# Performance work log

Hardware: AMD Instinct MI355X
Metric: run time of the kernel (lower is better)

Reference implementation:

```python
import jax, jax.numpy as jnp
import numpy as np

N, S, T, E, H = 4, 2048, 2048, 512, 8
HD = E // H  # head_dim = 64


def setup_inputs() -> dict:
    key0 = jax.random.key(0)
    ks = jax.random.split(key0, 12)
    sc = 1.0 / np.sqrt(E)
    inp = {
        "query": jax.random.normal(ks[0], (N, S, E), jnp.float32),
        "key": jax.random.normal(ks[1], (N, T, E), jnp.float32),
        "value": jax.random.normal(ks[2], (N, T, E), jnp.float32),
        "attn_mask": jnp.tril(jnp.ones((S, T), jnp.int32)),  # causal: 0 => masked
        # nn.Linear weights (out, in) and biases, torch convention y = x @ W.T + b
        "Wq": jax.random.normal(ks[3], (E, E), jnp.float32) * sc,
        "bq": jax.random.normal(ks[4], (E,), jnp.float32) * sc,
        "Wk": jax.random.normal(ks[5], (E, E), jnp.float32) * sc,
        "bk": jax.random.normal(ks[6], (E,), jnp.float32) * sc,
        "Wv": jax.random.normal(ks[7], (E, E), jnp.float32) * sc,
        "bv": jax.random.normal(ks[8], (E,), jnp.float32) * sc,
        "Wp": jax.random.normal(ks[9], (E, E), jnp.float32) * sc,
        "bp": jax.random.normal(ks[10], (E,), jnp.float32) * sc,
    }
    return inp


def reference(query, key, value, attn_mask, Wq, bq, Wk, bk, Wv, bv, Wp, bp):
    # QKV projections, split heads: (N, H, L, HD)
    q = (query @ Wq.T + bq).reshape(N, S, H, HD).transpose(0, 2, 1, 3)
    k = (key @ Wk.T + bk).reshape(N, T, H, HD).transpose(0, 2, 1, 3)
    v = (value @ Wv.T + bv).reshape(N, T, H, HD).transpose(0, 2, 1, 3)
    # scaled scores (N, H, S, T) -- intentionally materialized like the original
    e = jnp.einsum("nhsd,nhtd->nhst", q, k) / jnp.sqrt(jnp.float32(HD))
    e = jnp.where(attn_mask == 0, -jnp.inf, e)
    a = jax.nn.softmax(e, axis=-1)
    # dropout is identity in eval mode (reference runs deterministic/eval)
    y = jnp.einsum("nhst,nhtd->nhsd", a, v)
    y = y.transpose(0, 2, 1, 3).reshape(N, S, E)
    return y @ Wp.T + bp
```

## Files before the change

kernel.cpp:

```cpp
#include <hip/hip_runtime.h>


#define DEV __device__ __forceinline__

typedef unsigned short u16;
typedef unsigned int u32;
typedef __bf16 bf16x8 __attribute__((ext_vector_type(8)));
typedef float f32x4 __attribute__((ext_vector_type(4)));
typedef float f32x16 __attribute__((ext_vector_type(16)));

#define MFMA16(A, B, C) __builtin_amdgcn_mfma_f32_16x16x32_bf16(A, B, C, 0, 0, 0)
#define MFMA32(A, B, C) __builtin_amdgcn_mfma_f32_32x32x16_bf16(A, B, C, 0, 0, 0)

#define SC 0.18033688f

DEV u16 f2bf(float f) {
  u32 u = __builtin_bit_cast(u32, f);
  u += 0x7fffu + ((u >> 16) & 1u);
  return (u16)(u >> 16);
}
DEV u32 pk2(float lo, float hi) {
  u32 a = __builtin_bit_cast(u32, lo) + 0x8000u;
  u32 b = __builtin_bit_cast(u32, hi) + 0x8000u;
  return __builtin_amdgcn_perm(b, a, 0x07060302u);
}

DEV void cp16(void* l, const void* g) {
  __builtin_amdgcn_global_load_lds(
      (const __attribute__((address_space(1))) u32*)g,
      (__attribute__((address_space(3))) u32*)l, 16, 0, 0);
}

__global__ __launch_bounds__(256) void cast_all(
    const float* __restrict__ q, const float* __restrict__ k, const float* __restrict__ v,
    const float* __restrict__ wq, const float* __restrict__ wk, const float* __restrict__ wv,
    const float* __restrict__ wp,
    u16* qo, u16* ko, u16* vo, u16* wqo, u16* wko, u16* wvo, u16* wpo) {
  int b = blockIdx.x, tid = threadIdx.x;
  const float* s;
  u16* d;
  int off;
  float sc = 1.f;
  if (b < 12288) {
    int which = b >> 12;
    s = (which == 0) ? q : (which == 1) ? k : v;
    d = (which == 0) ? qo : (which == 1) ? ko : vo;
    off = (b & 4095) * 256;
  } else {
    int wb = b - 12288, which = wb >> 8;
    s = (which == 0) ? wq : (which == 1) ? wk : (which == 2) ? wv : wp;
    d = (which == 0) ? wqo : (which == 1) ? wko : (which == 2) ? wvo : wpo;
    off = (wb & 255) * 256;
    if (which == 0) sc = SC;
  }
  int i = off + tid;
  float4 f = ((const float4*)s)[i];
  ushort4 o;
  o.x = f2bf(f.x * sc); o.y = f2bf(f.y * sc); o.z = f2bf(f.z * sc); o.w = f2bf(f.w * sc);
  ((ushort4*)d)[i] = o;
}

DEV void gemm_loop(const u16* __restrict__ A, const u16* __restrict__ W,
                   u16* As, u16* Bs, int m0, int n0, int tid, f32x4 acc[4][4]) {
  const int lane = tid & 63, wid = tid >> 6;
  const int wm = wid & 1, wn = wid >> 1;
  const int l15 = lane & 15, l4 = lane >> 4;
  for (int kt = 0; kt < 512; kt += 32) {
    __syncthreads();
#pragma unroll
    for (int i = 0; i < 2; ++i) {
      int c = tid + 256 * i;
      int row = c >> 2, kc = (c & 3) * 8;
      cp16(&As[c * 8], A + (m0 + row) * 512 + kt + kc);
      cp16(&Bs[c * 8], W + (n0 + row) * 512 + kt + kc);
    }
    __syncthreads();
    bf16x8 af[4], bfr[4];
#pragma unroll
    for (int f = 0; f < 4; ++f) {
      af[f]  = *(const bf16x8*)&As[(wm * 64 + f * 16 + l15) * 32 + l4 * 8];
      bfr[f] = *(const bf16x8*)&Bs[(wn * 64 + f * 16 + l15) * 32 + l4 * 8];
    }
#pragma unroll
    for (int fm = 0; fm < 4; ++fm)
#pragma unroll
      for (int fn = 0; fn < 4; ++fn)
        acc[fm][fn] = MFMA16(af[fm], bfr[fn], acc[fm][fn]);
  }
}

__global__ __launch_bounds__(256) void gemm_qkv(
    const u16* __restrict__ qx, const u16* __restrict__ kx, const u16* __restrict__ vx,
    const u16* __restrict__ wq, const u16* __restrict__ wk, const u16* __restrict__ wv,
    const float* __restrict__ bq, const float* __restrict__ bk, const float* __restrict__ bv,
    u16* qp, u16* kp, u16* vt) {
  __shared__ u16 As[128 * 32];
  __shared__ u16 Bs[128 * 32];
  const int wsel = blockIdx.x >> 2;
  const int xq = blockIdx.x & 3;
  const u16* A = (wsel == 0) ? qx : (wsel == 1) ? kx : wv;
  const u16* W = (wsel == 0) ? wq : (wsel == 1) ? wk : vx;
  const float* bias = (wsel == 0) ? bq : (wsel == 1) ? bk : bv;
  const int m0 = (wsel == 2) ? xq * 128 : blockIdx.y * 128;
  const int n0 = (wsel == 2) ? blockIdx.y * 128 : xq * 128;
  const int tid = threadIdx.x, lane = tid & 63, wid = tid >> 6;
  const int wm = wid & 1, wn = wid >> 1;
  const int l15 = lane & 15, l4 = lane >> 4;

  f32x4 acc[4][4] = {};
  gemm_loop(A, W, As, Bs, m0, n0, tid, acc);

  if (wsel < 2) {
    u16* C = (wsel == 0) ? qp : kp;
    const float bscale = (wsel == 0) ? SC : 1.f;
#pragma unroll
    for (int fn = 0; fn < 4; ++fn) {
      int col = n0 + wn * 64 + fn * 16 + l15;
      float bvv = bias[col] * bscale;
#pragma unroll
      for (int fm = 0; fm < 4; ++fm) {
        int rowb = m0 + wm * 64 + fm * 16 + l4 * 4;
#pragma unroll
        for (int r = 0; r < 4; ++r)
          C[(rowb + r) * 512 + col] = f2bf(acc[fm][fn][r] + bvv);
      }
    }
  } else {
    const int nIdx = n0 >> 11;
    const int tb = n0 & 2047;
#pragma unroll
    for (int fm = 0; fm < 4; ++fm) {
      int rowb = m0 + wm * 64 + fm * 16 + l4 * 4;
#pragma unroll
      for (int r = 0; r < 4; ++r) {
        int row = rowb + r;
        float bvv = bias[row];
        int vtrow = (nIdx * 8 + (row >> 6)) * 64 + (row & 63);
#pragma unroll
        for (int fn = 0; fn < 4; ++fn) {
          int tcol = tb + wn * 64 + fn * 16 + l15;
          vt[vtrow * 2048 + tcol] = f2bf(acc[fm][fn][r] + bvv);
        }
      }
    }
  }
}

__global__ __launch_bounds__(256) void gemm_out(const u16* __restrict__ A,
                                                const u16* __restrict__ W,
                                                const float* __restrict__ bias,
                                                float* __restrict__ C) {
  __shared__ u16 As[128 * 32];
  __shared__ u16 Bs[128 * 32];
  const int n0 = blockIdx.x * 128, m0 = blockIdx.y * 128;
  const int tid = threadIdx.x, lane = tid & 63, wid = tid >> 6;
  const int wm = wid & 1, wn = wid >> 1;
  const int l15 = lane & 15, l4 = lane >> 4;

  f32x4 acc[4][4] = {};
  gemm_loop(A, W, As, Bs, m0, n0, tid, acc);

#pragma unroll
  for (int fn = 0; fn < 4; ++fn) {
    int col = n0 + wn * 64 + fn * 16 + l15;
    float bvv = bias[col];
#pragma unroll
    for (int fm = 0; fm < 4; ++fm) {
      int rowb = m0 + wm * 64 + fm * 16 + l4 * 4;
#pragma unroll
      for (int r = 0; r < 4; ++r)
        C[(rowb + r) * 512 + col] = acc[fm][fn][r] + bvv;
    }
  }
}

__global__ __launch_bounds__(128, 4) void attn_partial(
    const u16* __restrict__ Qg, const u16* __restrict__ Kg, const u16* __restrict__ Vt,
    u16* __restrict__ scrO, float* __restrict__ scrL) {
  __shared__ u16 Ks[128 * 64];
  __shared__ u16 Vs[64 * 128];

  const int nh = blockIdx.x;
  const int yy = blockIdx.y;
  const int qt = 31 - (yy >> 2), c = yy & 3;
  if (c > (qt >> 3)) return;
  const int n = nh >> 3, h = nh & 7;
  const int tid = threadIdx.x, lane = tid & 63, w = tid >> 6;
  const int l31 = lane & 31, lh = lane >> 5;
  const int s0 = qt * 64;
  const int ntiles = (qt >> 1) + 1;
  const int it0 = c * 4, it1 = min(it0 + 4, ntiles);

  const u16* Qb = Qg + (n * 2048 + s0) * 512 + h * 64;
  const u16* Kb = Kg + n * 2048 * 512 + h * 64;
  const u16* Vb = Vt + nh * 64 * 2048;

#pragma unroll
  for (int i = 0; i < 4; ++i) {
    int ci = tid + 128 * i;
    int m = ci >> 3, pc = ci & 7;
    cp16(&Ks[ci * 8], Qb + m * 512 + ((pc ^ (m & 7)) * 8));
  }
  __syncthreads();
  const int qm = w * 32 + l31;
  bf16x8 qf[4];
#pragma unroll
  for (int ks = 0; ks < 4; ++ks)
    qf[ks] = *(const bf16x8*)&Ks[qm * 64 + (((2 * ks + lh) ^ (qm & 7)) * 8)];

  f32x16 accO[2] = {};
  float lrow = 0.f;

  for (int it = it0; it < it1; ++it) {
    const int t0 = it * 128;
    __syncthreads();
#pragma unroll
    for (int i = 0; i < 8; ++i) {
      int ci = tid + 128 * i;
      int t = ci >> 3, pc = ci & 7;
      cp16(&Ks[ci * 8], Kb + (t0 + t) * 512 + ((pc ^ (t & 7)) * 8));
    }
#pragma unroll
    for (int i = 0; i < 8; ++i) {
      int ci = tid + 128 * i;
      int d = ci >> 4, pc = ci & 15;
      cp16(&Vs[ci * 8], Vb + d * 2048 + t0 + ((pc ^ (d & 15)) * 8));
    }
    __syncthreads();

    const bool diag = (it == ntiles - 1);
    const int nf = diag ? min(4, ((s0 + 32 * w + 31 - t0) >> 5) + 1) : 4;

#pragma unroll
    for (int f = 0; f < 4; ++f)
      if (f < nf) {
        f32x16 a = {};
        int tr = f * 32 + l31;
#pragma unroll
        for (int ks = 0; ks < 4; ++ks) {
          bf16x8 kf = *(const bf16x8*)&Ks[tr * 64 + (((2 * ks + lh) ^ (tr & 7)) * 8)];
          a = MFMA32(kf, qf[ks], a);
        }
        if (diag) {
#pragma unroll
          for (int rr = 0; rr < 16; ++rr) {
            int trow = t0 + f * 32 + (rr & 3) + 8 * (rr >> 2) + 4 * lh;
            a[rr] = (trow > s0 + qm) ? -1e30f : a[rr];
          }
        }
        u32 pd[8];
#pragma unroll
        for (int rr = 0; rr < 16; ++rr) {
          float pv = __builtin_amdgcn_exp2f(a[rr]);
          a[rr] = pv;
          lrow += pv;
        }
#pragma unroll
        for (int g = 0; g < 4; ++g) {
          pd[2 * g]     = pk2(a[4 * g + 0], a[4 * g + 1]);
          pd[2 * g + 1] = pk2(a[4 * g + 2], a[4 * g + 3]);
        }
#pragma unroll
        for (int hh = 0; hh < 2; ++hh) {
          u32 ss0 = lh ? pd[4 * hh + 0] : pd[4 * hh + 2];
          u32 ss1 = lh ? pd[4 * hh + 1] : pd[4 * hh + 3];
          u32 r0 = __shfl_xor(ss0, 32);
          u32 r1 = __shfl_xor(ss1, 32);
          uint4 b4;
          b4.x = lh ? r0 : pd[4 * hh + 0];
          b4.y = lh ? r1 : pd[4 * hh + 1];
          b4.z = lh ? pd[4 * hh + 2] : r0;
          b4.w = lh ? pd[4 * hh + 3] : r1;
          bf16x8 pb = __builtin_bit_cast(bf16x8, b4);
          const int ks = 2 * f + hh;
#pragma unroll
          for (int fd = 0; fd < 2; ++fd) {
            int d = fd * 32 + l31;
            bf16x8 vf = *(const bf16x8*)&Vs[d * 128 + (((2 * ks + lh) ^ (d & 15)) * 8)];
            accO[fd] = MFMA32(vf, pb, accO[fd]);
          }
        }
      }
  }

  lrow += __shfl_xor(lrow, 32);
  const int slot = ((nh << 5) + qt) * 4 + c;
  if (lh == 0) scrL[slot * 64 + qm] = lrow;
  u16* so = scrO + slot * 4096 + qm * 64;
#pragma unroll
  for (int fd = 0; fd < 2; ++fd)
#pragma unroll
    for (int g = 0; g < 4; ++g) {
      ushort4 o;
      o.x = f2bf(accO[fd][4 * g + 0]);
      o.y = f2bf(accO[fd][4 * g + 1]);
      o.z = f2bf(accO[fd][4 * g + 2]);
      o.w = f2bf(accO[fd][4 * g + 3]);
      *(ushort4*)(so + fd * 32 + 8 * g + 4 * lh) = o;
    }
}

__global__ __launch_bounds__(128) void attn_combine(const u16* __restrict__ scrO,
                                                    const float* __restrict__ scrL,
                                                    u16* __restrict__ y) {
  const int nh = blockIdx.x, qt = blockIdx.y;
  const int n = nh >> 3, h = nh & 7;
  const int nc = (qt >> 3) + 1;
  const int tid = threadIdx.x;
  const int m = tid >> 1, half = tid & 1;

  float o[32];
#pragma unroll
  for (int j = 0; j < 32; ++j) o[j] = 0.f;
  float lsum = 0.f;
  for (int cs = 0; cs < nc; ++cs) {
    int base = ((nh << 5) + qt) * 4 + cs;
    lsum += scrL[base * 64 + m];
    const uint4* p = (const uint4*)(scrO + base * 4096 + m * 64 + half * 32);
#pragma unroll
    for (int k2 = 0; k2 < 4; ++k2) {
      uint4 qv = p[k2];
      u32 ua[4] = {qv.x, qv.y, qv.z, qv.w};
#pragma unroll
      for (int j = 0; j < 4; ++j) {
        o[k2 * 8 + 2 * j]     += __builtin_bit_cast(float, ua[j] << 16);
        o[k2 * 8 + 2 * j + 1] += __builtin_bit_cast(float, ua[j] & 0xFFFF0000u);
      }
    }
  }
  float inv = 1.f / lsum;
  u16* yb = y + (n * 2048 + qt * 64 + m) * 512 + h * 64 + half * 32;
#pragma unroll
  for (int k2 = 0; k2 < 4; ++k2) {
    uint4 ov;
    ov.x = (u32)f2bf(o[k2 * 8 + 0] * inv) | ((u32)f2bf(o[k2 * 8 + 1] * inv) << 16);
    ov.y = (u32)f2bf(o[k2 * 8 + 2] * inv) | ((u32)f2bf(o[k2 * 8 + 3] * inv) << 16);
    ov.z = (u32)f2bf(o[k2 * 8 + 4] * inv) | ((u32)f2bf(o[k2 * 8 + 5] * inv) << 16);
    ov.w = (u32)f2bf(o[k2 * 8 + 6] * inv) | ((u32)f2bf(o[k2 * 8 + 7] * inv) << 16);
    *(uint4*)(yb + k2 * 8) = ov;
  }
}

extern "C" void kernel_launch(void* const* d_in, const int* in_sizes, int n_in,
                              void* d_out, int out_size, void* d_ws, size_t ws_size,
                              hipStream_t stream) {
  (void)in_sizes; (void)n_in; (void)out_size; (void)ws_size;
  const float* query = (const float*)d_in[0];
  const float* key_  = (const float*)d_in[1];
  const float* value = (const float*)d_in[2];
  const float* Wq = (const float*)d_in[4];
  const float* bq = (const float*)d_in[5];
  const float* Wk = (const float*)d_in[6];
  const float* bk = (const float*)d_in[7];
  const float* Wv = (const float*)d_in[8];
  const float* bv = (const float*)d_in[9];
  const float* Wp = (const float*)d_in[10];
  const float* bp = (const float*)d_in[11];

  char* ws = (char*)d_ws;
  u16* qx  = (u16*)(ws);
  u16* kx  = (u16*)(ws + 8388608);
  u16* vx  = (u16*)(ws + 16777216);
  u16* scrO = (u16*)(ws);
  u16* wqx = (u16*)(ws + 33554432);
  u16* wkx = (u16*)(ws + 34078720);
  u16* wvx = (u16*)(ws + 34603008);
  u16* wpx = (u16*)(ws + 35127296);
  u16* qp  = (u16*)(ws + 35651584);
  u16* kp  = (u16*)(ws + 44040192);
  u16* vt  = (u16*)(ws + 52428800);
  u16* y   = (u16*)(ws + 60817408);
  float* scrL = (float*)(ws + 69206016);

  cast_all<<<13312, 256, 0, stream>>>(query, key_, value, Wq, Wk, Wv, Wp,
                                      qx, kx, vx, wqx, wkx, wvx, wpx);
  gemm_qkv<<<dim3(12, 64), 256, 0, stream>>>(qx, kx, vx, wqx, wkx, wvx,
                                             bq, bk, bv, qp, kp, vt);
  attn_partial<<<dim3(32, 128), 128, 0, stream>>>(qp, kp, vt, scrO, scrL);
  attn_combine<<<dim3(32, 32), 128, 0, stream>>>(scrO, scrL, y);
  gemm_out<<<dim3(4, 64), 256, 0, stream>>>(y, wpx, bp, (float*)d_out);
}
```

Measured before the change: 215.9 us.

## Double-buffer K/V tiles and enlarge query tile to 128 rows in attention

The attention partial kernel now handles 128 query rows with 4 waves (256 threads), so each K/V tile loaded into shared memory is reused by twice as many queries. It double-buffers K/V in shared memory, prefetching the next tile while the current one is computed, and drops the second barrier per iteration. Block indexing is compacted so no empty blocks are launched, and the combine kernel is adjusted to the new slot layout. In exchange, shared memory per block grows to 64KB and there are fewer blocks, which may lower occupancy.

After: 213.1 us. Within noise of the previous version (-1.3%).

```diff
diff --git a/kernel.cpp b/kernel.cpp
--- a/kernel.cpp
+++ b/kernel.cpp
@@ -174,21 +174,23 @@
   }
 }
 
-__global__ __launch_bounds__(128, 4) void attn_partial(
+__global__ __launch_bounds__(256) void attn_partial(
     const u16* __restrict__ Qg, const u16* __restrict__ Kg, const u16* __restrict__ Vt,
     u16* __restrict__ scrO, float* __restrict__ scrL) {
-  __shared__ u16 Ks[128 * 64];
-  __shared__ u16 Vs[64 * 128];
+  __shared__ u16 KV[2][16384];
 
   const int nh = blockIdx.x;
-  const int yy = blockIdx.y;
-  const int qt = 31 - (yy >> 2), c = yy & 3;
-  if (c > (qt >> 3)) return;
+  const int j = blockIdx.y;
+  int qt, c;
+  if (j < 16)      { qt = 12 + (j >> 2); c = j & 3; }
+  else if (j < 28) { int r = j - 16; int q3 = r / 3; qt = 8 + q3; c = r - 3 * q3; }
+  else if (j < 36) { int r = j - 28; qt = 4 + (r >> 1); c = r & 1; }
+  else             { qt = j - 36; c = 0; }
   const int n = nh >> 3, h = nh & 7;
   const int tid = threadIdx.x, lane = tid & 63, w = tid >> 6;
   const int l31 = lane & 31, lh = lane >> 5;
-  const int s0 = qt * 64;
-  const int ntiles = (qt >> 1) + 1;
+  const int s0 = qt * 128;
+  const int ntiles = qt + 1;
   const int it0 = c * 4, it1 = min(it0 + 4, ntiles);
 
   const u16* Qb = Qg + (n * 2048 + s0) * 512 + h * 64;
@@ -197,39 +199,61 @@
 
 #pragma unroll
   for (int i = 0; i < 4; ++i) {
-    int ci = tid + 128 * i;
+    int ci = tid + 256 * i;
     int m = ci >> 3, pc = ci & 7;
-    cp16(&Ks[ci * 8], Qb + m * 512 + ((pc ^ (m & 7)) * 8));
+    cp16(&KV[1][ci * 8], Qb + m * 512 + ((pc ^ (m & 7)) * 8));
   }
   __syncthreads();
   const int qm = w * 32 + l31;
   bf16x8 qf[4];
 #pragma unroll
   for (int ks = 0; ks < 4; ++ks)
-    qf[ks] = *(const bf16x8*)&Ks[qm * 64 + (((2 * ks + lh) ^ (qm & 7)) * 8)];
+    qf[ks] = *(const bf16x8*)&KV[1][qm * 64 + (((2 * ks + lh) ^ (qm & 7)) * 8)];
+
+  {
+    const int t0 = it0 * 128;
+#pragma unroll
+    for (int i = 0; i < 4; ++i) {
+      int ci = tid + 256 * i;
+      int t = ci >> 3, pc = ci & 7;
+      cp16(&KV[0][ci * 8], Kb + (t0 + t) * 512 + ((pc ^ (t & 7)) * 8));
+    }
+#pragma unroll
+    for (int i = 0; i < 4; ++i) {
+      int ci = tid + 256 * i;
+      int d = ci >> 4, pc = ci & 15;
+      cp16(&KV[0][8192 + ci * 8], Vb + d * 2048 + t0 + ((pc ^ (d & 15)) * 8));
+    }
+  }
 
   f32x16 accO[2] = {};
   float lrow = 0.f;
 
   for (int it = it0; it < it1; ++it) {
+    const int b = (it - it0) & 1;
+    __syncthreads();
+    if (it + 1 < it1) {
+      const int t0n = (it + 1) * 128;
+      u16* Kd = KV[b ^ 1];
+      u16* Vd = KV[b ^ 1] + 8192;
+#pragma unroll
+      for (int i = 0; i < 4; ++i) {
+        int ci = tid + 256 * i;
+        int t = ci >> 3, pc = ci & 7;
+        cp16(&Kd[ci * 8], Kb + (t0n + t) * 512 + ((pc ^ (t & 7)) * 8));
+      }
+#pragma unroll
+      for (int i = 0; i < 4; ++i) {
+        int ci = tid + 256 * i;
+        int d = ci >> 4, pc = ci & 15;
+        cp16(&Vd[ci * 8], Vb + d * 2048 + t0n + ((pc ^ (d & 15)) * 8));
+      }
+    }
+    const u16* Ks = KV[b];
+    const u16* Vs = KV[b] + 8192;
     const int t0 = it * 128;
-    __syncthreads();
-#pragma unroll
-    for (int i = 0; i < 8; ++i) {
-      int ci = tid + 128 * i;
-      int t = ci >> 3, pc = ci & 7;
-      cp16(&Ks[ci * 8], Kb + (t0 + t) * 512 + ((pc ^ (t & 7)) * 8));
-    }
-#pragma unroll
-    for (int i = 0; i < 8; ++i) {
-      int ci = tid + 128 * i;
-      int d = ci >> 4, pc = ci & 15;
-      cp16(&Vs[ci * 8], Vb + d * 2048 + t0 + ((pc ^ (d & 15)) * 8));
-    }
-    __syncthreads();
-
     const bool diag = (it == ntiles - 1);
-    const int nf = diag ? min(4, ((s0 + 32 * w + 31 - t0) >> 5) + 1) : 4;
+    const int nf = diag ? (w + 1) : 4;
 
 #pragma unroll
     for (int f = 0; f < 4; ++f)
@@ -241,7 +265,7 @@
           bf16x8 kf = *(const bf16x8*)&Ks[tr * 64 + (((2 * ks + lh) ^ (tr & 7)) * 8)];
           a = MFMA32(kf, qf[ks], a);
         }
-        if (diag) {
+        if (diag && f == w) {
 #pragma unroll
           for (int rr = 0; rr < 16; ++rr) {
             int trow = t0 + f * 32 + (rr & 3) + 8 * (rr >> 2) + 4 * lh;
@@ -284,9 +308,9 @@
   }
 
   lrow += __shfl_xor(lrow, 32);
-  const int slot = ((nh << 5) + qt) * 4 + c;
-  if (lh == 0) scrL[slot * 64 + qm] = lrow;
-  u16* so = scrO + slot * 4096 + qm * 64;
+  const int slot = ((nh << 4) + qt) * 4 + c;
+  if (lh == 0) scrL[slot * 128 + qm] = lrow;
+  u16* so = scrO + slot * 8192 + qm * 64;
 #pragma unroll
   for (int fd = 0; fd < 2; ++fd)
 #pragma unroll
@@ -300,36 +324,36 @@
     }
 }
 
-__global__ __launch_bounds__(128) void attn_combine(const u16* __restrict__ scrO,
+__global__ __launch_bounds__(256) void attn_combine(const u16* __restrict__ scrO,
                                                     const float* __restrict__ scrL,
                                                     u16* __restrict__ y) {
   const int nh = blockIdx.x, qt = blockIdx.y;
   const int n = nh >> 3, h = nh & 7;
-  const int nc = (qt >> 3) + 1;
+  const int nc = (qt >> 2) + 1;
   const int tid = threadIdx.x;
   const int m = tid >> 1, half = tid & 1;
 
   float o[32];
 #pragma unroll
-  for (int j = 0; j < 32; ++j) o[j] = 0.f;
+  for (int jj = 0; jj < 32; ++jj) o[jj] = 0.f;
   float lsum = 0.f;
   for (int cs = 0; cs < nc; ++cs) {
-    int base = ((nh << 5) + qt) * 4 + cs;
-    lsum += scrL[base * 64 + m];
-    const uint4* p = (const uint4*)(scrO + base * 4096 + m * 64 + half * 32);
+    int base = ((nh << 4) + qt) * 4 + cs;
+    lsum += scrL[base * 128 + m];
+    const uint4* p = (const uint4*)(scrO + base * 8192 + m * 64 + half * 32);
 #pragma unroll
     for (int k2 = 0; k2 < 4; ++k2) {
       uint4 qv = p[k2];
       u32 ua[4] = {qv.x, qv.y, qv.z, qv.w};
 #pragma unroll
-      for (int j = 0; j < 4; ++j) {
-        o[k2 * 8 + 2 * j]     += __builtin_bit_cast(float, ua[j] << 16);
-        o[k2 * 8 + 2 * j + 1] += __builtin_bit_cast(float, ua[j] & 0xFFFF0000u);
+      for (int jj = 0; jj < 4; ++jj) {
+        o[k2 * 8 + 2 * jj]     += __builtin_bit_cast(float, ua[jj] << 16);
+        o[k2 * 8 + 2 * jj + 1] += __builtin_bit_cast(float, ua[jj] & 0xFFFF0000u);
       }
     }
   }
   float inv = 1.f / lsum;
-  u16* yb = y + (n * 2048 + qt * 64 + m) * 512 + h * 64 + half * 32;
+  u16* yb = y + (n * 2048 + qt * 128 + m) * 512 + h * 64 + half * 32;
 #pragma unroll
   for (int k2 = 0; k2 < 4; ++k2) {
     uint4 ov;
@@ -376,7 +400,7 @@
                                       qx, kx, vx, wqx, wkx, wvx, wpx);
   gemm_qkv<<<dim3(12, 64), 256, 0, stream>>>(qx, kx, vx, wqx, wkx, wvx,
                                              bq, bk, bv, qp, kp, vt);
-  attn_partial<<<dim3(32, 128), 128, 0, stream>>>(qp, kp, vt, scrO, scrL);
-  attn_combine<<<dim3(32, 32), 128, 0, stream>>>(scrO, scrL, y);
+  attn_partial<<<dim3(32, 40), 256, 0, stream>>>(qp, kp, vt, scrO, scrL);
+  attn_combine<<<dim3(32, 16), 256, 0, stream>>>(scrO, scrL, y);
   gemm_out<<<dim3(4, 64), 256, 0, stream>>>(y, wpx, bp, (float*)d_out);
 }
```
